# Performance work log

Hardware: AMD Instinct MI355X
Metric: run time of the kernel (lower is better)

Reference implementation:

```python
import jax, jax.numpy as jnp
import numpy as np

FISTA_ITER = 50
LAMBDA = 0.1
POWER_ITER = 100


def power_method(W):
    # Estimates c = largest eigenvalue of W^T W (squared spectral norm).
    # Torch code uses a random init vector; we use a fixed key for determinism.
    X0 = jax.random.normal(jax.random.key(1), (1, W.shape[1]), dtype=W.dtype)

    def body(i, carry):
        X, _ = carry
        X = (X @ W.T) @ W            # [1, m]
        nm = jnp.linalg.norm(X)
        return (X / nm, nm)

    _, nm = jax.lax.fori_loop(0, POWER_ITER, body, (X0, jnp.asarray(1.0, W.dtype)))
    return nm


def soft_threshold(X, lam):
    return jnp.sign(X) * jax.nn.relu(jnp.abs(X) - lam)


def fista(Y, W, lam, iters):
    c = power_method(W)
    eta = 1.0 / c
    Gamma0 = soft_threshold(Y @ (eta * W), lam)   # [B, m]
    Y_norm = jnp.linalg.norm(Y)
    t0 = jnp.asarray(1.0, Y.dtype)

    def step(carry, _):
        Gamma, Z, t = carry
        residual = Z @ W.T - Y                                   # [B, n]
        Gamma_new = soft_threshold(Z - eta * (residual @ W), lam / c)
        t_new = (1.0 + jnp.sqrt(1.0 + 4.0 * t ** 2)) / 2.0
        Z_new = Gamma_new + (t - 1.0) / t_new * (Gamma_new - Gamma)
        nrm = jnp.linalg.norm(residual) / Y_norm
        return (Gamma_new, Z_new, t_new), nrm

    (Gamma, _, _), norms = jax.lax.scan(step, (Gamma0, Gamma0, t0), None, length=iters)
    return Gamma, norms


def setup_inputs() -> dict:
    key = jax.random.key(0)
    k1, k2 = jax.random.split(key)
    Y = jax.random.normal(k1, (8192, 784), dtype=jnp.float32)
    W = jax.random.normal(k2, (784, 2048), dtype=jnp.float32)
    W = W / jnp.linalg.norm(W, axis=0, keepdims=True)  # NormDict
    return {"Y": Y, "W": W}


def reference(Y, W):
    Gamma, norms = fista(Y, W, LAMBDA, FISTA_ITER)
    X = Gamma @ W.T                  # reconstruction [B, 784]
    return (X, Gamma, norms)
```

## Files before the change

kernel.cpp:

```cpp
#include <hip/hip_runtime.h>
#include <math.h>

#define B_DIM   8192
#define N_DIM   784
#define NPAD    800
#define NROWS_W 1024
#define M_DIM   2048
#define XSZ     (B_DIM*N_DIM)
#define GSZ     (B_DIM*M_DIM)
#define NITER   50
#define PITER   100

typedef __attribute__((ext_vector_type(8))) short short8;
typedef __attribute__((ext_vector_type(4))) float floatx4;

__device__ __forceinline__ void async_ld16(const unsigned short* g, unsigned short* l){
  __builtin_amdgcn_global_load_lds(
      (const __attribute__((address_space(1))) unsigned int*)g,
      (__attribute__((address_space(3))) unsigned int*)l,
      16, 0, 0);
}

__device__ __forceinline__ unsigned rotl32(unsigned x, int d){ return (x<<d)|(x>>(32-d)); }

__device__ void threefry2x32(unsigned& v0, unsigned& v1){
  const unsigned ks0=0u, ks1=1u, ks2=0x1BD11BDBu;
  unsigned x0=v0+ks0, x1=v1+ks1;
#define RND(R) { x0+=x1; x1=rotl32(x1,R); x1^=x0; }
  RND(13) RND(15) RND(26) RND(6)
  x0+=ks1; x1+=ks2+1u;
  RND(17) RND(29) RND(16) RND(24)
  x0+=ks2; x1+=ks0+2u;
  RND(13) RND(15) RND(26) RND(6)
  x0+=ks0; x1+=ks1+3u;
  RND(17) RND(29) RND(16) RND(24)
  x0+=ks1; x1+=ks2+4u;
  RND(13) RND(15) RND(26) RND(6)
  x0+=ks2; x1+=ks0+5u;
#undef RND
  v0=x0; v1=x1;
}

__device__ float erfinv_f(float x){
  float w = -logf((1.0f-x)*(1.0f+x));
  float p;
  if (w < 5.0f){
    w -= 2.5f;
    p = 2.81022636e-08f;
    p = fmaf(p,w, 3.43273939e-07f);
    p = fmaf(p,w,-3.5233877e-06f);
    p = fmaf(p,w,-4.39150654e-06f);
    p = fmaf(p,w, 0.00021858087f);
    p = fmaf(p,w,-0.00125372503f);
    p = fmaf(p,w,-0.00417768164f);
    p = fmaf(p,w, 0.246640727f);
    p = fmaf(p,w, 1.50140941f);
  } else {
    w = sqrtf(w) - 3.0f;
    p = -0.000200214257f;
    p = fmaf(p,w, 0.000100950558f);
    p = fmaf(p,w, 0.00134934322f);
    p = fmaf(p,w,-0.00367342844f);
    p = fmaf(p,w, 0.00573950773f);
    p = fmaf(p,w,-0.0076224613f);
    p = fmaf(p,w, 0.00943887047f);
    p = fmaf(p,w, 1.00167406f);
    p = fmaf(p,w, 2.83297682f);
  }
  return p*x;
}

__device__ float bits_to_normal(unsigned b){
  unsigned fb = (b>>9) | 0x3f800000u;
  float u01 = __uint_as_float(fb) - 1.0f;
  const float lo = -0.99999994f;
  float u = u01*(1.0f - lo) + lo;
  u = fmaxf(lo, u);
  return 1.41421356237f * erfinv_f(u);
}

__global__ void setup_kernel(float* __restrict__ xbuf0, float* __restrict__ accs,
                             float* __restrict__ dbuf){
  int i = threadIdx.x;
  if (i < 64) accs[i] = 0.0f;
  if (i < 128) dbuf[i] = (i==0) ? 1.0f : 0.0f;
  unsigned v0 = (unsigned)i, v1 = (unsigned)(1024+i);
  threefry2x32(v0, v1);
  xbuf0[i]        = bits_to_normal(v0);
  xbuf0[1024 + i] = bits_to_normal(v1);
}

__device__ __forceinline__ unsigned short f2bf(float f){
  unsigned u = __float_as_uint(f);
  unsigned r = (u + 0x7fffu + ((u>>16)&1u)) >> 16;
  return (unsigned short)r;
}
__device__ __forceinline__ unsigned pack2(float a, float b){
  return (unsigned)f2bf(a) | ((unsigned)f2bf(b) << 16);
}
__device__ __forceinline__ float bf2f(unsigned short s){
  return __uint_as_float(((unsigned)s) << 16);
}

__global__ void conv_w(const float* __restrict__ W, unsigned short* __restrict__ Wbf){
  int i4 = (blockIdx.x*256 + threadIdx.x)*4;
  int row = i4 >> 11;
  uint2 p = make_uint2(0,0);
  if (row < N_DIM){
    float4 v = *(const float4*)(W + (size_t)row*M_DIM + (i4 & 2047));
    p.x = pack2(v.x, v.y); p.y = pack2(v.z, v.w);
  }
  *(uint2*)(Wbf + i4) = p;
}

__global__ void conv_y(const float* __restrict__ Y, unsigned short* __restrict__ Ybf){
  int row = blockIdx.x;
  int c4 = threadIdx.x*4;
  if (c4 >= NPAD) return;
  uint2 p = make_uint2(0,0);
  if (c4 < N_DIM){
    float4 v = *(const float4*)(Y + (size_t)row*N_DIM + c4);
    p.x = pack2(v.x, v.y); p.y = pack2(v.z, v.w);
  }
  *(uint2*)(Ybf + (size_t)row*NPAD + c4) = p;
}

__global__ void transpose_w(const float* __restrict__ W, unsigned short* __restrict__ WTbf){
  __shared__ float tile[32][33];
  int k0 = blockIdx.x*32;
  int j0 = blockIdx.y*32;
  int tx = threadIdx.x & 31, ty = threadIdx.x >> 5;
#pragma unroll
  for (int i=0;i<4;i++){
    int j = j0 + ty + 8*i;
    float v = (j < N_DIM) ? W[(size_t)j*M_DIM + k0 + tx] : 0.0f;
    tile[tx][ty+8*i] = v;
  }
  __syncthreads();
#pragma unroll
  for (int i=0;i<4;i++){
    int k = k0 + ty + 8*i;
    WTbf[(size_t)k*NPAD + j0 + tx] = f2bf(tile[ty+8*i][tx]);
  }
}

__global__ __launch_bounds__(256)
void compute_qp(const float* __restrict__ W, float* __restrict__ Qp){
  __shared__ float As2[64][33];
  __shared__ float Bs2[64][33];
  const int t = threadIdx.x;
  const int a0 = blockIdx.x*64, b0 = blockIdx.y*64;
  const int ty = t>>4, tx = t&15;
  float acc[4][4];
#pragma unroll
  for (int i=0;i<4;i++)
#pragma unroll
    for (int j=0;j<4;j++) acc[i][j]=0.0f;

  for (int k0=0; k0<M_DIM; k0+=32){
#pragma unroll
    for (int h=0; h<2; ++h){
      int row = h*32 + (t>>3);
      int kq  = (t&7)*4;
      float4 av = make_float4(0,0,0,0), bv = make_float4(0,0,0,0);
      if (a0+row < N_DIM) av = *(const float4*)(W + (size_t)(a0+row)*M_DIM + k0 + kq);
      if (b0+row < N_DIM) bv = *(const float4*)(W + (size_t)(b0+row)*M_DIM + k0 + kq);
      As2[row][kq]=av.x; As2[row][kq+1]=av.y; As2[row][kq+2]=av.z; As2[row][kq+3]=av.w;
      Bs2[row][kq]=bv.x; Bs2[row][kq+1]=bv.y; Bs2[row][kq+2]=bv.z; Bs2[row][kq+3]=bv.w;
    }
    __syncthreads();
#pragma unroll
    for (int kk=0; kk<32; ++kk){
      float a[4], b[4];
#pragma unroll
      for (int i=0;i<4;i++) a[i] = As2[ty*4+i][kk];
#pragma unroll
      for (int j=0;j<4;j++) b[j] = Bs2[tx*4+j][kk];
#pragma unroll
      for (int i=0;i<4;i++)
#pragma unroll
        for (int j=0;j<4;j++) acc[i][j] = fmaf(a[i], b[j], acc[i][j]);
    }
    __syncthreads();
  }
#pragma unroll
  for (int i=0;i<4;i++){
    int a = a0 + ty*4 + i;
    if (a >= N_DIM) continue;
#pragma unroll
    for (int j=0;j<4;j++){
      int b = b0 + tx*4 + j;
      if (b < N_DIM) Qp[(size_t)a*N_DIM + b] = acc[i][j];
    }
  }
}

__global__ void u0_kernel(const float* __restrict__ x0, const float* __restrict__ W,
                          float* __restrict__ u0){
  int wave = threadIdx.x>>6, lane = threadIdx.x&63;
  int j = blockIdx.x*4 + wave;
  const float* Wr = W + (size_t)j*M_DIM;
  float s = 0.0f;
  for (int k=lane; k<M_DIM; k+=64) s = fmaf(x0[k], Wr[k], s);
  for (int off=32; off>0; off>>=1) s += __shfl_down(s, off);
  if (lane==0) u0[j] = s;
}

__global__ void pm_qp(const float* __restrict__ vin, const float* __restrict__ din,
                      const float* __restrict__ Qp,
                      float* __restrict__ vout, float* __restrict__ dout){
  int wave = threadIdx.x>>6, lane = threadIdx.x&63;
  int j = blockIdx.x*4 + wave;
  float inv = 1.0f/sqrtf(*din);
  const float* Qr = Qp + (size_t)j*N_DIM;
  float s = 0.0f;
  for (int k=lane; k<N_DIM; k+=64) s = fmaf(vin[k], Qr[k], s);
  for (int off=32; off>0; off>>=1) s += __shfl_down(s, off);
  if (lane==0){
    float w = s * inv;
    vout[j] = w;
    atomicAdd(dout, w * vin[j] * inv);
  }
}

__global__ void finish_power2(const float* __restrict__ d100, const float* __restrict__ accs,
                              float* __restrict__ params){
  float c = sqrtf(*d100);
  params[0] = c;
  params[1] = 1.0f/c;
  params[2] = 0.1f/c;
  params[3] = sqrtf(accs[0]);
}

__global__ void sumsq_kernel(const float* __restrict__ v, int n, float* __restrict__ acc){
  __shared__ float red[256];
  int t = threadIdx.x;
  float s = 0.0f;
  for (int i = blockIdx.x*256 + t; i < n; i += gridDim.x*256){ float x = v[i]; s = fmaf(x,x,s); }
  red[t] = s; __syncthreads();
  for (int off=128; off>0; off>>=1){ if (t<off) red[t]+=red[t+off]; __syncthreads(); }
  if (t==0) atomicAdd(acc, red[0]);
}

__device__ __forceinline__ float softthr(float v, float th){
  float a = fmaxf(fabsf(v) - th, 0.0f);
  return copysignf(a, v);
}

template<int MODE>
__global__ __launch_bounds__(256)
void mfma_nt(const unsigned short* __restrict__ Abf,
             const unsigned short* __restrict__ Bbf,
             const float* __restrict__ Y,
             unsigned short* __restrict__ Rbf,
             float* __restrict__ X,
             float* __restrict__ nacc){
  __shared__ float4 smem4[2560];
  unsigned short* As0 = (unsigned short*)smem4;
  unsigned short* Bs0 = As0 + 64*32;
  unsigned short* As1 = Bs0 + 256*32;
  unsigned short* Bs1 = As1 + 64*32;
  float* fbuf = (float*)smem4;

  const int bid = blockIdx.x;
  const int g8  = bid & 7, w = bid >> 3;
  const int m0  = (g8*16 + (w>>2))*64;
  const int n0  = (w & 3)*256;

  const int t    = threadIdx.x;
  const int wave = t>>6, lane = t&63;
  const int wm2  = wave>>1, wn2 = wave&1;
  const int quad = lane>>4, l15 = lane&15;
  const int lrow = lane>>2;
  const int lks  = ((lane&3) ^ ((lrow>>1)&3))*8;
  const int ksw  = (quad ^ ((l15>>1)&3))*8;

  floatx4 acc[2][8];
#pragma unroll
  for (int i=0;i<2;i++)
#pragma unroll
    for (int j=0;j<8;j++) acc[i][j] = (floatx4)(0.0f);

  auto stage = [&](unsigned short* As, unsigned short* Bs, int k0){
    async_ld16(Abf + (size_t)(m0 + wave*16 + lrow)*M_DIM + k0 + lks, &As[wave*512]);
#pragma unroll
    for (int c=0; c<4; ++c){
      int chunk = wave*4 + c;
      async_ld16(Bbf + (size_t)(n0 + chunk*16 + lrow)*M_DIM + k0 + lks, &Bs[chunk*512]);
    }
  };

  stage(As0, Bs0, 0);
  __syncthreads();
  int cur = 0;
  for (int k0=0; k0<M_DIM; k0+=32, cur^=1){
    unsigned short* As = cur ? As1 : As0;
    unsigned short* Bs = cur ? Bs1 : Bs0;
    if (k0+32 < M_DIM) stage(cur ? As0 : As1, cur ? Bs0 : Bs1, k0+32);
    short8 af[2], bfr[8];
#pragma unroll
    for (int ti=0; ti<2; ++ti)
      af[ti] = *(const short8*)&As[(wm2*32 + ti*16 + l15)*32 + ksw];
#pragma unroll
    for (int tj=0; tj<8; ++tj)
      bfr[tj] = *(const short8*)&Bs[(wn2*128 + tj*16 + l15)*32 + ksw];
#pragma unroll
    for (int ti=0; ti<2; ++ti)
#pragma unroll
      for (int tj=0; tj<8; ++tj)
        acc[ti][tj] = __builtin_amdgcn_mfma_f32_16x16x32_bf16(af[ti], bfr[tj], acc[ti][tj], 0, 0, 0);
    __syncthreads();
  }

  float ss = 0.0f;
#pragma unroll
  for (int c=0; c<4; ++c){
    if (wn2 == (c>>1)){
      int tb = (c&1)*4;
#pragma unroll
      for (int ti=0; ti<2; ++ti)
#pragma unroll
        for (int u=0; u<4; ++u)
#pragma unroll
          for (int r=0; r<4; ++r)
            fbuf[(wm2*32 + ti*16 + quad*4 + r)*68 + u*16 + l15] = acc[ti][tb+u][r];
    }
    __syncthreads();
#pragma unroll
    for (int k=0; k<4; ++k){
      int row = k*16 + (t>>4);
      int col = (t&15)*4;
      int m = m0 + row;
      int n = n0 + c*64 + col;
      float4 v = *(const float4*)&fbuf[row*68 + col];
      if (MODE==0){
        if (n < N_DIM){
          float4 yv = *(const float4*)(Y + (size_t)m*N_DIM + n);
          float r0 = v.x - yv.x, r1 = v.y - yv.y, r2 = v.z - yv.z, r3 = v.w - yv.w;
          uint2 p; p.x = pack2(r0, r1); p.y = pack2(r2, r3);
          *(uint2*)(Rbf + (size_t)m*NPAD + n) = p;
          ss = fmaf(r0,r0, fmaf(r1,r1, fmaf(r2,r2, fmaf(r3,r3, ss))));
        } else if (n < NPAD){
          *(uint2*)(Rbf + (size_t)m*NPAD + n) = make_uint2(0,0);
        }
      } else {
        if (n < N_DIM) *(float4*)(X + (size_t)m*N_DIM + n) = v;
      }
    }
    __syncthreads();
  }

  if (MODE==0){
    for (int off=32; off>0; off>>=1) ss += __shfl_down(ss, off);
    if (lane==0) atomicAdd(nacc, ss);
  }
}

template<int MODE>
__global__ __launch_bounds__(256,3)
void mfma_nn(const unsigned short* __restrict__ Abf,
             const unsigned short* __restrict__ WTbf,
             float* __restrict__ Gamma,
             unsigned short* __restrict__ Zhi,
             float* __restrict__ Zf,
             float* __restrict__ Gf,
             const float* __restrict__ params,
             float mu){
  __shared__ float4 smem4[2048];
  unsigned short* As0 = (unsigned short*)smem4;
  unsigned short* Bs0 = As0 + 128*32;
  unsigned short* As1 = Bs0 + 128*32;
  unsigned short* Bs1 = As1 + 128*32;
  float* fbuf = (float*)smem4;

  const int bid = blockIdx.x;
  const int g8  = bid & 7, w = bid >> 3;
  const int m0  = (g8*8 + (w>>4))*128;
  const int n0  = (w & 15)*128;

  const int t    = threadIdx.x;
  const int wave = t>>6, lane = t&63;
  const int wm   = wave>>1, wn = wave&1;
  const int quad = lane>>4, l15 = lane&15;
  const int lrow = lane>>2;
  const int lks  = ((lane&3) ^ ((lrow>>1)&3))*8;
  const int ksw  = (quad ^ ((l15>>1)&3))*8;

  floatx4 acc[4][4];
#pragma unroll
  for (int i=0;i<4;i++)
#pragma unroll
    for (int j=0;j<4;j++) acc[i][j] = (floatx4)(0.0f);

  auto stage = [&](unsigned short* As, unsigned short* Bs, int k0){
#pragma unroll
    for (int c=0; c<2; ++c){
      int chunk = wave*2 + c;
      async_ld16(Abf  + (size_t)(m0 + chunk*16 + lrow)*NPAD + k0 + lks, &As[chunk*512]);
      async_ld16(WTbf + (size_t)(n0 + chunk*16 + lrow)*NPAD + k0 + lks, &Bs[chunk*512]);
    }
  };

  stage(As0, Bs0, 0);
  __syncthreads();
  int cur = 0;
  for (int k0=0; k0<NPAD; k0+=32, cur^=1){
    unsigned short* As = cur ? As1 : As0;
    unsigned short* Bs = cur ? Bs1 : Bs0;
    if (k0+32 < NPAD) stage(cur ? As0 : As1, cur ? Bs0 : Bs1, k0+32);
    short8 af[4], bfr[4];
#pragma unroll
    for (int ti=0; ti<4; ++ti)
      af[ti] = *(const short8*)&As[(wm*64 + ti*16 + l15)*32 + ksw];
#pragma unroll
    for (int tj=0; tj<4; ++tj)
      bfr[tj] = *(const short8*)&Bs[(wn*64 + tj*16 + l15)*32 + ksw];
#pragma unroll
    for (int ti=0; ti<4; ++ti)
#pragma unroll
      for (int tj=0; tj<4; ++tj)
        acc[ti][tj] = __builtin_amdgcn_mfma_f32_16x16x32_bf16(af[ti], bfr[tj], acc[ti][tj], 0, 0, 0);
    __syncthreads();
  }

  const float eta  = params[1];
  const float lamc = params[2];
  const size_t blockL = (size_t)((m0>>7)*16 + (n0>>7));
  float* GfB = Gf + blockL*16384 + (size_t)t*4;
  float* ZfB = Zf + blockL*16384 + (size_t)t*4;
  const int mrow0 = m0 + wm*64 + quad*4;
  const int ncol  = n0 + wn*64 + l15;

  if (MODE==2){
#pragma unroll
    for (int ti=0; ti<4; ++ti)
#pragma unroll
      for (int tj=0; tj<4; ++tj){
        float4 zf4 = *(const float4*)(ZfB + (ti*4+tj)*1024);
        acc[ti][tj][0] = softthr(zf4.x - eta*acc[ti][tj][0], lamc);
        acc[ti][tj][1] = softthr(zf4.y - eta*acc[ti][tj][1], lamc);
        acc[ti][tj][2] = softthr(zf4.z - eta*acc[ti][tj][2], lamc);
        acc[ti][tj][3] = softthr(zf4.w - eta*acc[ti][tj][3], lamc);
      }
    __syncthreads();
#pragma unroll
    for (int c=0; c<4; ++c){
      if (wn == (c>>1)){
        int tb = (c&1)*2;
#pragma unroll
        for (int ti=0; ti<4; ++ti)
#pragma unroll
          for (int u=0; u<2; ++u)
#pragma unroll
            for (int r=0; r<4; ++r)
              fbuf[(wm*64 + ti*16 + quad*4 + r)*36 + u*16 + l15] = acc[ti][tb+u][r];
      }
      __syncthreads();
#pragma unroll
      for (int k=0; k<4; ++k){
        int row = k*32 + (t>>3);
        int col = (t&7)*4;
        int m = m0 + row;
        int n = n0 + c*32 + col;
        size_t idx = (size_t)m*M_DIM + n;
        float4 g4 = *(const float4*)&fbuf[row*36 + col];
        *(float4*)(Gamma + idx) = g4;
        uint2 phx; phx.x = pack2(g4.x, g4.y); phx.y = pack2(g4.z, g4.w);
        *(uint2*)(Zhi + idx) = phx;
      }
      __syncthreads();
    }
  } else {
#pragma unroll
    for (int ti=0; ti<4; ++ti){
      float4 go4[4], zf4[4];
      if (MODE==1){
#pragma unroll
        for (int tj=0; tj<4; ++tj) go4[tj] = *(const float4*)(GfB + (ti*4+tj)*1024);
#pragma unroll
        for (int tj=0; tj<4; ++tj) zf4[tj] = *(const float4*)(ZfB + (ti*4+tj)*1024);
      }
#pragma unroll
      for (int tj=0; tj<4; ++tj){
        float gr[4], zn[4];
        if (MODE==1){
          float z[4]  = {zf4[tj].x, zf4[tj].y, zf4[tj].z, zf4[tj].w};
          float go[4] = {go4[tj].x, go4[tj].y, go4[tj].z, go4[tj].w};
#pragma unroll
          for (int r=0;r<4;r++){
            gr[r] = softthr(z[r] - eta*acc[ti][tj][r], lamc);
            zn[r] = gr[r] + mu*(gr[r] - go[r]);
          }
        } else {
#pragma unroll
          for (int r=0;r<4;r++){ gr[r] = softthr(eta*acc[ti][tj][r], 0.1f); zn[r] = gr[r]; }
        }
        *(float4*)(GfB + (ti*4+tj)*1024) = make_float4(gr[0],gr[1],gr[2],gr[3]);
        *(float4*)(ZfB + (ti*4+tj)*1024) = make_float4(zn[0],zn[1],zn[2],zn[3]);
        size_t zb = (size_t)(mrow0 + ti*16)*M_DIM + ncol + tj*16;
        Zhi[zb]            = f2bf(zn[0]);
        Zhi[zb + M_DIM]    = f2bf(zn[1]);
        Zhi[zb + 2*M_DIM]  = f2bf(zn[2]);
        Zhi[zb + 3*M_DIM]  = f2bf(zn[3]);
      }
    }
  }
}

__global__ void norms_finalize(const float* __restrict__ nacc, const float* __restrict__ params,
                               float* __restrict__ out){
  int i = threadIdx.x;
  if (i < NITER) out[i] = sqrtf(nacc[i]) / params[3];
}

extern "C" void kernel_launch(void* const* d_in, const int* in_sizes, int n_in,
                              void* d_out, int out_size, void* d_ws, size_t ws_size,
                              hipStream_t stream){
  const float* Y  = (const float*)d_in[0];
  const float* W  = (const float*)d_in[1];
  float* out      = (float*)d_out;
  float* X        = out;
  float* Gamma    = out + XSZ;
  float* norms    = out + XSZ + GSZ;

  unsigned short* Zhi  = (unsigned short*)d_ws;
  float* Zf            = (float*)(Zhi + (size_t)GSZ);
  unsigned short* Rbf  = (unsigned short*)(Zf + (size_t)GSZ);
  unsigned short* Wbf  = Rbf  + (size_t)B_DIM*NPAD;
  unsigned short* WTbf = Wbf  + (size_t)NROWS_W*M_DIM;
  float* Qp     = (float*)(WTbf + (size_t)M_DIM*NPAD);
  float* w0     = Qp + (size_t)N_DIM*N_DIM;
  float* w1     = w0 + 1024;
  float* dbuf   = w1 + 1024;
  float* params = dbuf + 128;
  float* accs   = params + 8;
  float* xb0    = accs + 64;

  float* Gf = Gamma;

  setup_kernel<<<dim3(1), dim3(1024), 0, stream>>>(xb0, accs, dbuf);
  sumsq_kernel<<<dim3(512), dim3(256), 0, stream>>>(Y, XSZ, accs);
  conv_w      <<<dim3(2048), dim3(256), 0, stream>>>(W, Wbf);
  transpose_w <<<dim3(64,25), dim3(256), 0, stream>>>(W, WTbf);
  conv_y      <<<dim3(B_DIM), dim3(256), 0, stream>>>(Y, Rbf);

  compute_qp<<<dim3(13,13), dim3(256), 0, stream>>>(W, Qp);
  u0_kernel <<<dim3(196), dim3(256), 0, stream>>>(xb0, W, w0);
  float* va = w0; float* vb = w1;
  for (int it=1; it<=PITER; ++it){
    pm_qp<<<dim3(196), dim3(256), 0, stream>>>(va, dbuf + it - 1, Qp, vb, dbuf + it);
    float* tmp = va; va = vb; vb = tmp;
  }
  finish_power2<<<dim3(1), dim3(1), 0, stream>>>(dbuf + PITER, accs, params);

  mfma_nn<0><<<dim3(1024), dim3(256), 0, stream>>>(Rbf, WTbf, Gamma, Zhi, Zf, Gf, params, 0.0f);

  float tcur = 1.0f;
  for (int it=0; it<NITER; ++it){
    mfma_nt<0><<<dim3(512), dim3(256), 0, stream>>>(Zhi, Wbf, Y, Rbf, nullptr, accs + 1 + it);
    float tsq = tcur*tcur;
    float tn  = (1.0f + sqrtf(1.0f + 4.0f*tsq)) / 2.0f;
    float mu  = (tcur - 1.0f) / tn;
    tcur = tn;
    if (it < NITER-1)
      mfma_nn<1><<<dim3(1024), dim3(256), 0, stream>>>(Rbf, WTbf, Gamma, Zhi, Zf, Gf, params, mu);
    else
      mfma_nn<2><<<dim3(1024), dim3(256), 0, stream>>>(Rbf, WTbf, Gamma, Zhi, Zf, Gf, params, mu);
  }

  norms_finalize<<<dim3(1), dim3(64), 0, stream>>>(accs + 1, params, norms);

  mfma_nt<1><<<dim3(512), dim3(256), 0, stream>>>(Zhi, Wbf, nullptr, nullptr, X, nullptr);
}
```

Before: 8.931 ms.

## Split-K the W·Wᵀ Gram kernel, drop LDS swizzle, stage bf16 Z stores via LDS

The Gram matrix kernel now splits the 2048-long reduction into 8 slices over a third grid dimension and accumulates with atomicAdd into a pre-zeroed buffer. This gives 13x13x8 blocks instead of 169, so more of the GPU is used. Separately, the XOR swizzle on LDS tile offsets in both MFMA kernels is removed in favour of plain linear offsets, which may bring back bank conflicts. The epilogue of the NN MFMA kernel now writes bf16 Z values into a padded LDS tile and then stores full 16-byte rows, replacing scattered 2-byte global stores. That costs an extra barrier and a larger shared allocation.

```diff
diff --git a/kernel.cpp b/kernel.cpp
--- a/kernel.cpp
+++ b/kernel.cpp
@@ -144,12 +144,23 @@
   }
 }
 
+__global__ void zero_qp(float* __restrict__ Qp){
+  int i = (blockIdx.x*256 + threadIdx.x)*4;
+  if (i < N_DIM*N_DIM){
+    Qp[i] = 0.0f;
+    if (i+1 < N_DIM*N_DIM) Qp[i+1] = 0.0f;
+    if (i+2 < N_DIM*N_DIM) Qp[i+2] = 0.0f;
+    if (i+3 < N_DIM*N_DIM) Qp[i+3] = 0.0f;
+  }
+}
+
 __global__ __launch_bounds__(256)
 void compute_qp(const float* __restrict__ W, float* __restrict__ Qp){
   __shared__ float As2[64][33];
   __shared__ float Bs2[64][33];
   const int t = threadIdx.x;
   const int a0 = blockIdx.x*64, b0 = blockIdx.y*64;
+  const int kbase = blockIdx.z*256;
   const int ty = t>>4, tx = t&15;
   float acc[4][4];
 #pragma unroll
@@ -157,7 +168,7 @@
 #pragma unroll
     for (int j=0;j<4;j++) acc[i][j]=0.0f;
 
-  for (int k0=0; k0<M_DIM; k0+=32){
+  for (int k0=kbase; k0<kbase+256; k0+=32){
 #pragma unroll
     for (int h=0; h<2; ++h){
       int row = h*32 + (t>>3);
@@ -190,7 +201,7 @@
 #pragma unroll
     for (int j=0;j<4;j++){
       int b = b0 + tx*4 + j;
-      if (b < N_DIM) Qp[(size_t)a*N_DIM + b] = acc[i][j];
+      if (b < N_DIM) atomicAdd(&Qp[(size_t)a*N_DIM + b], acc[i][j]);
     }
   }
 }
@@ -272,8 +283,7 @@
   const int wm2  = wave>>1, wn2 = wave&1;
   const int quad = lane>>4, l15 = lane&15;
   const int lrow = lane>>2;
-  const int lks  = ((lane&3) ^ ((lrow>>1)&3))*8;
-  const int ksw  = (quad ^ ((l15>>1)&3))*8;
+  const int lk   = (lane&3)*8;
 
   floatx4 acc[2][8];
 #pragma unroll
@@ -282,11 +292,11 @@
     for (int j=0;j<8;j++) acc[i][j] = (floatx4)(0.0f);
 
   auto stage = [&](unsigned short* As, unsigned short* Bs, int k0){
-    async_ld16(Abf + (size_t)(m0 + wave*16 + lrow)*M_DIM + k0 + lks, &As[wave*512]);
+    async_ld16(Abf + (size_t)(m0 + wave*16 + lrow)*M_DIM + k0 + lk, &As[wave*512]);
 #pragma unroll
     for (int c=0; c<4; ++c){
       int chunk = wave*4 + c;
-      async_ld16(Bbf + (size_t)(n0 + chunk*16 + lrow)*M_DIM + k0 + lks, &Bs[chunk*512]);
+      async_ld16(Bbf + (size_t)(n0 + chunk*16 + lrow)*M_DIM + k0 + lk, &Bs[chunk*512]);
     }
   };
 
@@ -300,10 +310,10 @@
     short8 af[2], bfr[8];
 #pragma unroll
     for (int ti=0; ti<2; ++ti)
-      af[ti] = *(const short8*)&As[(wm2*32 + ti*16 + l15)*32 + ksw];
+      af[ti] = *(const short8*)&As[(wm2*32 + ti*16 + l15)*32 + quad*8];
 #pragma unroll
     for (int tj=0; tj<8; ++tj)
-      bfr[tj] = *(const short8*)&Bs[(wn2*128 + tj*16 + l15)*32 + ksw];
+      bfr[tj] = *(const short8*)&Bs[(wn2*128 + tj*16 + l15)*32 + quad*8];
 #pragma unroll
     for (int ti=0; ti<2; ++ti)
 #pragma unroll
@@ -366,12 +376,13 @@
              float* __restrict__ Gf,
              const float* __restrict__ params,
              float mu){
-  __shared__ float4 smem4[2048];
-  unsigned short* As0 = (unsigned short*)smem4;
+  __shared__ uint4 smemu[2176];
+  unsigned short* As0 = (unsigned short*)smemu;
   unsigned short* Bs0 = As0 + 128*32;
   unsigned short* As1 = Bs0 + 128*32;
   unsigned short* Bs1 = As1 + 128*32;
-  float* fbuf = (float*)smem4;
+  unsigned short* zbuf = (unsigned short*)smemu;
+  float* fbuf = (float*)smemu;
 
   const int bid = blockIdx.x;
   const int g8  = bid & 7, w = bid >> 3;
@@ -383,8 +394,7 @@
   const int wm   = wave>>1, wn = wave&1;
   const int quad = lane>>4, l15 = lane&15;
   const int lrow = lane>>2;
-  const int lks  = ((lane&3) ^ ((lrow>>1)&3))*8;
-  const int ksw  = (quad ^ ((l15>>1)&3))*8;
+  const int lk   = (lane&3)*8;
 
   floatx4 acc[4][4];
 #pragma unroll
@@ -396,8 +406,8 @@
 #pragma unroll
     for (int c=0; c<2; ++c){
       int chunk = wave*2 + c;
-      async_ld16(Abf  + (size_t)(m0 + chunk*16 + lrow)*NPAD + k0 + lks, &As[chunk*512]);
-      async_ld16(WTbf + (size_t)(n0 + chunk*16 + lrow)*NPAD + k0 + lks, &Bs[chunk*512]);
+      async_ld16(Abf  + (size_t)(m0 + chunk*16 + lrow)*NPAD + k0 + lk, &As[chunk*512]);
+      async_ld16(WTbf + (size_t)(n0 + chunk*16 + lrow)*NPAD + k0 + lk, &Bs[chunk*512]);
     }
   };
 
@@ -411,10 +421,10 @@
     short8 af[4], bfr[4];
 #pragma unroll
     for (int ti=0; ti<4; ++ti)
-      af[ti] = *(const short8*)&As[(wm*64 + ti*16 + l15)*32 + ksw];
+      af[ti] = *(const short8*)&As[(wm*64 + ti*16 + l15)*32 + quad*8];
 #pragma unroll
     for (int tj=0; tj<4; ++tj)
-      bfr[tj] = *(const short8*)&Bs[(wn*64 + tj*16 + l15)*32 + ksw];
+      bfr[tj] = *(const short8*)&Bs[(wn*64 + tj*16 + l15)*32 + quad*8];
 #pragma unroll
     for (int ti=0; ti<4; ++ti)
 #pragma unroll
@@ -428,8 +438,8 @@
   const size_t blockL = (size_t)((m0>>7)*16 + (n0>>7));
   float* GfB = Gf + blockL*16384 + (size_t)t*4;
   float* ZfB = Zf + blockL*16384 + (size_t)t*4;
-  const int mrow0 = m0 + wm*64 + quad*4;
-  const int ncol  = n0 + wn*64 + l15;
+  const int row0 = wm*64 + quad*4;
+  const int col0 = wn*64 + l15;
 
   if (MODE==2){
 #pragma unroll
@@ -473,12 +483,12 @@
   } else {
 #pragma unroll
     for (int ti=0; ti<4; ++ti){
-      float4 go4[4], zf4[4];
+      float4 zf4[4], go4[4];
       if (MODE==1){
 #pragma unroll
+        for (int tj=0; tj<4; ++tj) zf4[tj] = *(const float4*)(ZfB + (ti*4+tj)*1024);
+#pragma unroll
         for (int tj=0; tj<4; ++tj) go4[tj] = *(const float4*)(GfB + (ti*4+tj)*1024);
-#pragma unroll
-        for (int tj=0; tj<4; ++tj) zf4[tj] = *(const float4*)(ZfB + (ti*4+tj)*1024);
       }
 #pragma unroll
       for (int tj=0; tj<4; ++tj){
@@ -497,12 +507,20 @@
         }
         *(float4*)(GfB + (ti*4+tj)*1024) = make_float4(gr[0],gr[1],gr[2],gr[3]);
         *(float4*)(ZfB + (ti*4+tj)*1024) = make_float4(zn[0],zn[1],zn[2],zn[3]);
-        size_t zb = (size_t)(mrow0 + ti*16)*M_DIM + ncol + tj*16;
-        Zhi[zb]            = f2bf(zn[0]);
-        Zhi[zb + M_DIM]    = f2bf(zn[1]);
-        Zhi[zb + 2*M_DIM]  = f2bf(zn[2]);
-        Zhi[zb + 3*M_DIM]  = f2bf(zn[3]);
+        int lr = row0 + ti*16;
+        int lc = col0 + tj*16;
+#pragma unroll
+        for (int r=0;r<4;r++) zbuf[(lr+r)*136 + lc] = f2bf(zn[r]);
       }
+    }
+    __syncthreads();
+    const int srow = t>>4;
+    const int scol = (t&15)*8;
+#pragma unroll
+    for (int p=0; p<8; ++p){
+      int row = p*16 + srow;
+      uint4 v = *(const uint4*)&zbuf[row*136 + scol];
+      *(uint4*)(Zhi + (size_t)(m0+row)*M_DIM + n0 + scol) = v;
     }
   }
 }
@@ -544,7 +562,8 @@
   transpose_w <<<dim3(64,25), dim3(256), 0, stream>>>(W, WTbf);
   conv_y      <<<dim3(B_DIM), dim3(256), 0, stream>>>(Y, Rbf);
 
-  compute_qp<<<dim3(13,13), dim3(256), 0, stream>>>(W, Qp);
+  zero_qp   <<<dim3(601), dim3(256), 0, stream>>>(Qp);
+  compute_qp<<<dim3(13,13,8), dim3(256), 0, stream>>>(W, Qp);
   u0_kernel <<<dim3(196), dim3(256), 0, stream>>>(xb0, W, w0);
   float* va = w0; float* vb = w1;
   for (int it=1; it<=PITER; ++it){
```

New measurement: 9.143 ms. 2.4% more time.
